# Kernel optimization log

Hardware: AMD Instinct MI355X
Metric: run time of the kernel (lower is better)

Reference implementation:

```python
import jax, jax.numpy as jnp
import numpy as np
from jax.scipy.special import logsumexp

REG = 0.1
ITERS = 10
TEMP = 0.1
W = 0.5            # cross_domain_weight
NEG = -1000000.0   # mask fill value used by the torch module
EPS = 1e-12        # F.normalize eps


def setup_inputs() -> dict:
    key = jax.random.key(0)
    k1, k2, k3, k4, k5 = jax.random.split(key, 5)
    n, n_ex, m, L, h = 64, 4, 49, 32, 512
    x = jax.random.normal(k1, (n * n_ex, m, h), jnp.float32)
    y = jax.random.normal(k2, (n, L, h), jnp.float32)
    lengths = jax.random.randint(k3, (n,), 8, L + 1)
    y_mask = jnp.arange(L)[None, :] >= lengths[:, None]  # True = padded token
    dustbin_im = 0.1 * jax.random.normal(k4, (1, 1, 1), jnp.float32)
    dustbin_lang = 0.1 * jax.random.normal(k5, (1, 1, 1), jnp.float32)
    return {"x": x, "y": y, "dustbin_im": dustbin_im,
            "dustbin_lang": dustbin_lang, "y_mask": y_mask}


def _l2norm(t):
    return t / jnp.maximum(jnp.linalg.norm(t, axis=-1, keepdims=True), EPS)


def _log_sinkhorn(Z, log_mu, log_nu, mask_cols, iters, reg):
    # Z: (b, m+1, n+1); mask_cols: (b, n+1) bool, True = invalid column
    u = jnp.zeros_like(log_mu)
    v = jnp.where(mask_cols, NEG, jnp.zeros_like(log_nu))
    pen = mask_cols[:, None, :].astype(Z.dtype) * 1e6

    def body(carry, _):
        u, v = carry
        M = (Z + u[:, :, None] + v[:, None, :]) / reg
        u = u + reg * (log_mu - logsumexp(M, axis=2))
        M = (Z + u[:, :, None] + v[:, None, :]) / reg
        v_new = v + reg * (log_nu - logsumexp(M + pen, axis=1))
        v = jnp.where(mask_cols, NEG, v_new)
        return (u, v), None

    (u, v), _ = jax.lax.scan(body, (u, v), None, length=iters)
    return (Z + u[:, :, None] + v[:, None, :]) / reg


def reference(x, y, dustbin_im, dustbin_lang, y_mask):
    n, L, h = y.shape
    n_ex = x.shape[0] // n
    m = x.shape[1]
    b = n * n * n_ex

    xn = _l2norm(x)   # (n*n_ex, m, h)
    yn = _l2norm(y)   # (n, L, h)
    # equivalent to repeat_interleave(x, n) vs repeat(y, n*n_ex): index i*n + j
    scores = jnp.einsum('imh,jlh->ijml', xn, yn).reshape(b, m, L)

    mask_cols = jnp.tile(y_mask, (n * n_ex, 1))                       # (b, L)
    mask_cols = jnp.concatenate([mask_cols, jnp.zeros((b, 1), bool)], axis=1)  # (b, L+1)
    scores_mask = jnp.broadcast_to(mask_cols[:, None, :], (b, m + 1, L + 1))

    a_im = jnp.clip(dustbin_im, -1.0, 1.0)
    a_lang = jnp.clip(dustbin_lang, -1.0, 1.0)
    bins0 = jnp.broadcast_to(a_im, (b, m, 1))
    bins1 = jnp.broadcast_to(a_lang, (b, 1, L))
    alpha = jnp.broadcast_to(a_im, (b, 1, 1))
    couplings = jnp.concatenate(
        [jnp.concatenate([scores, bins0], axis=2),
         jnp.concatenate([bins1, alpha], axis=2)], axis=1)            # (b, m+1, L+1)
    couplings = jnp.where(scores_mask, NEG, couplings)

    ms = jnp.asarray(m, scores.dtype)
    ns = (~scores_mask).sum(axis=(1, 2)).astype(scores.dtype) / (m + 1) - 1  # valid tokens per row
    norm = -jnp.log(ms + ns)                                          # (b,)
    log_mu = jnp.concatenate(
        [jnp.broadcast_to(norm[:, None], (b, m)), (jnp.log(ns) + norm)[:, None]], axis=1)
    log_nu = jnp.concatenate(
        [jnp.broadcast_to(norm[:, None], (b, L)), (jnp.log(ms) + norm)[:, None]], axis=1)
    log_nu = jnp.where(mask_cols, NEG, log_nu)

    Zlog = _log_sinkhorn(couplings, log_mu, log_nu, mask_cols, ITERS, REG)
    Zm = jnp.exp(Zlog - norm[:, None, None])                          # transport plan
    ot_scores = (scores * Zm[:, :-1, :-1]).sum(axis=(1, 2)) / TEMP    # (b,)

    scores2 = ot_scores.reshape(n * n_ex, n)
    matching = Zm.reshape(n * n_ex, n, m + 1, L + 1)

    idx = jnp.arange(n * n_ex)
    grp = idx // n_ex                                                 # lang index of image i
    pos = scores2[idx, grp]                                           # (n*n_ex,)
    # InfoNCE by language: pos vs all other langs for each image (full row)
    loss_lang = -(pos - logsumexp(scores2, axis=1)).mean()
    # InfoNCE by image: pos vs out-of-group images for the same lang
    cols = scores2.T[grp]                                             # (n*n_ex, n*n_ex), row i = scores2[:, grp[i]]
    allowed = (idx[None, :] // n_ex != grp[:, None]) | (idx[None, :] == idx[:, None])
    lse_im = logsumexp(jnp.where(allowed, cols, -jnp.inf), axis=1)
    loss_im = -(pos - lse_im).mean()
    loss = W * loss_lang + (1.0 - W) * loss_im
    return matching, loss
```

## Files before the change

kernel.cpp:

```cpp
#include <hip/hip_runtime.h>
#include <math.h>

#define XROWS 12544
#define YROWS 2048
#define HD 512
#define NM 49
#define NL 32
#define MP1 50
#define LP1 33
#define BSTRIDE 1650
#define INVREG 10.0f
#define ZSTR 1652

typedef __attribute__((ext_vector_type(8))) short short8;
typedef __attribute__((ext_vector_type(4))) float floatx4;
typedef _Float16 half2_t __attribute__((ext_vector_type(2)));

__device__ __forceinline__ unsigned short f2bf(float f) {
    unsigned int u = __builtin_bit_cast(unsigned int, f);
    u = (u + 0x7FFFu + ((u >> 16) & 1u)) >> 16;
    return (unsigned short)u;
}
__device__ __forceinline__ unsigned short f16b(float v) {
    return __builtin_bit_cast(unsigned short, (_Float16)v);
}

__device__ __forceinline__ void gload_lds16(const void* g, void* l) {
    typedef const __attribute__((address_space(1))) unsigned int* gp_t;
    typedef __attribute__((address_space(3))) unsigned int* lp_t;
    __builtin_amdgcn_global_load_lds((gp_t)g, (lp_t)l, 16, 0, 0);
}

__device__ __forceinline__ float rl(float v, int l) {
    return __builtin_bit_cast(float, __builtin_amdgcn_readlane(__builtin_bit_cast(int, v), l));
}
__device__ __forceinline__ half2_t rlh2(unsigned v, int l) {
    return __builtin_bit_cast(half2_t, (unsigned)__builtin_amdgcn_readlane((int)v, l));
}
__device__ __forceinline__ float fdot2(half2_t a, half2_t b, float c) {
    return __builtin_amdgcn_fdot2(a, b, c, false);
}

__global__ __launch_bounds__(256) void normcvt_kernel(
    const float* __restrict__ x, const float* __restrict__ y,
    unsigned short* __restrict__ xb, unsigned short* __restrict__ yb)
{
    const int wid = blockIdx.x * 4 + (threadIdx.x >> 6);
    const int lane = threadIdx.x & 63;
    if (wid >= XROWS + YROWS) return;
    const float* src;
    unsigned short* dst;
    if (wid < XROWS) { src = x + (size_t)wid * HD;           dst = xb + (size_t)wid * HD; }
    else             { src = y + (size_t)(wid - XROWS) * HD; dst = yb + (size_t)(wid - XROWS) * HD; }
    const float4 v0 = *(const float4*)(src + lane * 8);
    const float4 v1 = *(const float4*)(src + lane * 8 + 4);
    float s = v0.x*v0.x + v0.y*v0.y + v0.z*v0.z + v0.w*v0.w
            + v1.x*v1.x + v1.y*v1.y + v1.z*v1.z + v1.w*v1.w;
    #pragma unroll
    for (int o = 32; o > 0; o >>= 1) s += __shfl_xor(s, o, 64);
    const float inv = 1.0f / fmaxf(sqrtf(s), 1e-12f);
    short8 ov;
    ov[0] = (short)f2bf(v0.x * inv); ov[1] = (short)f2bf(v0.y * inv);
    ov[2] = (short)f2bf(v0.z * inv); ov[3] = (short)f2bf(v0.w * inv);
    ov[4] = (short)f2bf(v1.x * inv); ov[5] = (short)f2bf(v1.y * inv);
    ov[6] = (short)f2bf(v1.z * inv); ov[7] = (short)f2bf(v1.w * inv);
    *(short8*)(dst + lane * 8) = ov;
}

__global__ __launch_bounds__(512) void fused_kernel(
    const unsigned short* __restrict__ xb, const unsigned short* __restrict__ yb,
    const int* __restrict__ ymask,
    const float* __restrict__ d_im, const float* __restrict__ d_lang,
    float* __restrict__ outZ, float* __restrict__ scores2)
{
    const int wv   = threadIdx.x >> 6;
    const int lane = threadIdx.x & 63;
    const int i  = blockIdx.x & 255;
    const int jg = blockIdx.x >> 8;
    const int j  = jg * 8 + wv;
    const int pair = i * 64 + j;
    __shared__ alignas(16) float LDSU[8 * ZSTR];
    char* XSB = (char*)LDSU;
    float* zs = LDSU + wv * ZSTR;
    float* base = outZ + (size_t)pair * BSTRIDE;

    #pragma unroll
    for (int pass = 0; pass < 7; ++pass) {
        const int row = pass * 8 + wv;
        if (row < NM)
            gload_lds16(xb + ((size_t)i * NM + row) * HD + lane * 8, XSB + row * 1040);
    }
    __syncthreads();

    const int mval = (lane < NL) ? (ymask[j * NL + lane] != 0) : 1;
    const unsigned long long vbm = __ballot(lane < NL && !mval);
    const float ns = (float)__popcll(vbm);
    const float kim   = __expf(fminf(fmaxf(d_im[0],   -1.f), 1.f) * INVREG);
    const float klang = __expf(fminf(fmaxf(d_lang[0], -1.f), 1.f) * INVREG);

    const int la = lane & 15;
    const int koff = (lane >> 4) * 8;
    const unsigned short* yr0 = yb + ((size_t)j * NL + la) * HD + koff;
    const unsigned short* yr1 = yr0 + 16 * HD;

    floatx4 acc[4][2] = {};
    #pragma unroll
    for (int kt = 0; kt < 16; ++kt) {
        const int kb = (kt * 32 + koff) * 2;
        const short8 a0 = *(const short8*)(XSB + (0  + la) * 1040 + kb);
        const short8 a1 = *(const short8*)(XSB + (16 + la) * 1040 + kb);
        const short8 a2 = *(const short8*)(XSB + (32 + la) * 1040 + kb);
        const short8 a3 = *(const short8*)(XSB + 48 * 1040 + kb);
        const short8 b0 = *(const short8*)(yr0 + kt * 32);
        const short8 b1 = *(const short8*)(yr1 + kt * 32);
        acc[0][0] = __builtin_amdgcn_mfma_f32_16x16x32_bf16(a0, b0, acc[0][0], 0, 0, 0);
        acc[0][1] = __builtin_amdgcn_mfma_f32_16x16x32_bf16(a0, b1, acc[0][1], 0, 0, 0);
        acc[1][0] = __builtin_amdgcn_mfma_f32_16x16x32_bf16(a1, b0, acc[1][0], 0, 0, 0);
        acc[1][1] = __builtin_amdgcn_mfma_f32_16x16x32_bf16(a1, b1, acc[1][1], 0, 0, 0);
        acc[2][0] = __builtin_amdgcn_mfma_f32_16x16x32_bf16(a2, b0, acc[2][0], 0, 0, 0);
        acc[2][1] = __builtin_amdgcn_mfma_f32_16x16x32_bf16(a2, b1, acc[2][1], 0, 0, 0);
        acc[3][0] = __builtin_amdgcn_mfma_f32_16x16x32_bf16(a3, b0, acc[3][0], 0, 0, 0);
        acc[3][1] = __builtin_amdgcn_mfma_f32_16x16x32_bf16(a3, b1, acc[3][1], 0, 0, 0);
    }
    __syncthreads();

    unsigned short* T = (unsigned short*)zs;
    const bool mA = (vbm >> la) & 1ull;
    const bool mB = (vbm >> (16 + la)) & 1ull;
    float kA[16], kB[16];
    #pragma unroll
    for (int mi = 0; mi < 3; ++mi)
        #pragma unroll
        for (int q = 0; q < 4; ++q) {
            kA[mi*4+q] = mA ? __expf(acc[mi][0][q] * INVREG) : 0.f;
            kB[mi*4+q] = mB ? __expf(acc[mi][1][q] * INVREG) : 0.f;
        }
    kA[12] = mA ? __expf(acc[3][0][0] * INVREG) : 0.f;
    kB[12] = mB ? __expf(acc[3][1][0] * INVREG) : 0.f;
    kA[13] = kA[14] = kA[15] = 0.f;
    kB[13] = kB[14] = kB[15] = 0.f;

    #pragma unroll
    for (int mi = 0; mi < 3; ++mi) {
        const int r0 = mi * 16 + ((lane >> 4) << 2);
        ushort4 wa, wb;
        wa.x = f16b(kA[mi*4+0]); wa.y = f16b(kA[mi*4+1]);
        wa.z = f16b(kA[mi*4+2]); wa.w = f16b(kA[mi*4+3]);
        wb.x = f16b(kB[mi*4+0]); wb.y = f16b(kB[mi*4+1]);
        wb.z = f16b(kB[mi*4+2]); wb.w = f16b(kB[mi*4+3]);
        *(ushort4*)(T + la * 52 + r0)        = wa;
        *(ushort4*)(T + (16 + la) * 52 + r0) = wb;
    }
    if ((lane >> 4) == 0) {
        T[la * 52 + 48]        = f16b(kA[12]);
        T[(16 + la) * 52 + 48] = f16b(kB[12]);
    }
    if (lane < NL)       T[lane * 52 + 49] = f16b(((vbm >> lane) & 1ull) ? klang : 0.f);
    else if (lane == NL) T[32 * 52 + 49]   = f16b(kim);
    if (lane < NM)       T[32 * 52 + lane] = f16b(kim);
    asm volatile("s_waitcnt lgkmcnt(0)" ::: "memory");
    __builtin_amdgcn_sched_barrier(0);

    half2_t kr2[17];
    {
        const int p = (lane < MP1) ? lane : 0;
        #pragma unroll
        for (int q = 0; q < 16; ++q) {
            const unsigned lo = T[(2*q)   * 52 + p];
            const unsigned hi = T[(2*q+1) * 52 + p];
            kr2[q] = __builtin_bit_cast(half2_t, lo | (hi << 16));
        }
        half2_t h; h[0] = (_Float16)kim; h[1] = (_Float16)0.f;
        kr2[16] = h;
    }
    half2_t kc2[25];
    {
        const int tb = ((lane < LP1) ? lane : 0) * 52;
        #pragma unroll
        for (int q = 0; q < 25; ++q)
            kc2[q] = __builtin_bit_cast(half2_t, *(const unsigned*)(T + tb + 2*q));
    }

    const float mup = (lane < NM) ? 1.f : ns;
    const float nup = (lane < NL) ? 1.f : 49.f;
    const bool colA = (lane < NL) ? (((vbm >> lane) & 1ull) != 0ull) : (lane == NL);
    float eu = 0.f;
    float ev = colA ? 1.f : 0.f;

    for (int it = 0; it < 10; ++it) {
        const float evn = __shfl_xor(ev, 1, 64);
        const auto evp_ = __builtin_amdgcn_cvt_pkrtz(ev, evn);
        const unsigned evpu = __builtin_bit_cast(unsigned, evp_);
        float a0 = 0.f, a1 = 0.f;
        #pragma unroll
        for (int q = 0; q < 17; q += 2) {
            a0 = fdot2(kr2[q], rlh2(evpu, 2*q), a0);
            if (q + 1 < 17) a1 = fdot2(kr2[q+1], rlh2(evpu, 2*q+2), a1);
        }
        eu = __fdividef(mup, a0 + a1);

        const float eun = __shfl_xor(eu, 1, 64);
        const auto eup_ = __builtin_amdgcn_cvt_pkrtz(eu, eun);
        const unsigned eupu = __builtin_bit_cast(unsigned, eup_);
        float b0 = 0.f, b1 = 0.f;
        #pragma unroll
        for (int q = 0; q < 25; q += 2) {
            b0 = fdot2(kc2[q], rlh2(eupu, 2*q), b0);
            if (q + 1 < 25) b1 = fdot2(kc2[q+1], rlh2(eupu, 2*q+2), b1);
        }
        const float Sv = b0 + b1;
        ev = colA ? __fdividef(nup, Sv) : 0.f;
    }

    const float ev32 = rl(ev, 32);
    const float eu49 = rl(eu, 49);
    const float evA  = __shfl(ev, la, 64);
    const float evB  = __shfl(ev, 16 + la, 64);
    float ot = 0.f;
    #pragma unroll
    for (int mi = 0; mi < 4; ++mi) {
        #pragma unroll
        for (int q = 0; q < 4; ++q) {
            const int row = mi * 16 + ((lane >> 4) << 2) + q;
            const float eur = __shfl(eu, row, 64);
            if (row < NM) {
                const float s0 = acc[mi][0][q];
                const float s1 = acc[mi][1][q];
                const float zm0 = kA[mi*4+q] * eur * evA;
                const float zm1 = kB[mi*4+q] * eur * evB;
                zs[row * 33 + la]      = zm0;
                zs[row * 33 + 16 + la] = zm1;
                ot = fmaf(s0 * INVREG, zm0, fmaf(s1 * INVREG, zm1, ot));
            }
        }
    }
    if (lane < MP1) zs[lane * 33 + 32] = kim * eu * ev32;
    if (lane < LP1) {
        const float kd = (lane < NL) ? (((vbm >> lane) & 1ull) ? klang : 0.f) : kim;
        zs[NM * 33 + lane] = kd * eu49 * ev;
    }
    #pragma unroll
    for (int o = 32; o > 0; o >>= 1) ot += __shfl_xor(ot, o, 64);
    if (lane == 0) scores2[pair] = ot;
    asm volatile("s_waitcnt lgkmcnt(0)" ::: "memory");
    __builtin_amdgcn_sched_barrier(0);
    #pragma unroll
    for (int t = 0; t < 13; ++t) {
        const int idx = t * 64 + lane;
        if (idx < 825) *(float2*)(base + idx * 2) = *(const float2*)&zs[idx * 2];
    }
}

__global__ __launch_bounds__(256) void loss_kernel(
    const float* __restrict__ s2, float* __restrict__ out)
{
    __shared__ float S2[16384];
    __shared__ float colmax[64], colsum[64];
    __shared__ float wred[4];
    const int tid = threadIdx.x;
    for (int t = tid; t < 4096; t += 256)
        ((float4*)S2)[t] = ((const float4*)s2)[t];
    __syncthreads();

    const int gc = tid >> 2, sc = tid & 3;
    float cm = -3.0e38f;
    for (int k = sc * 64; k < sc * 64 + 64; ++k) cm = fmaxf(cm, S2[k * 64 + gc]);
    cm = fmaxf(cm, __shfl_xor(cm, 1, 64));
    cm = fmaxf(cm, __shfl_xor(cm, 2, 64));
    float cs = 0.f;
    for (int k = sc * 64; k < sc * 64 + 64; ++k)
        if ((k >> 2) != gc) cs += __expf(S2[k * 64 + gc] - cm);
    cs += __shfl_xor(cs, 1, 64);
    cs += __shfl_xor(cs, 2, 64);
    if (sc == 0) { colmax[gc] = cm; colsum[gc] = cs; }
    __syncthreads();

    const int i = tid;
    const int g = i >> 2;
    const float pos = S2[i * 64 + g];
    float mx = -3.0e38f;
    for (int jj = 0; jj < 64; ++jj) {
        const int c = (jj + i) & 63;
        mx = fmaxf(mx, S2[i * 64 + c]);
    }
    float sm = 0.f;
    for (int jj = 0; jj < 64; ++jj) {
        const int c = (jj + i) & 63;
        sm += __expf(S2[i * 64 + c] - mx);
    }
    const float lse1 = __logf(sm) + mx;

    const float cmg = colmax[g], csg = colsum[g];
    const float lse2 = __logf(csg + __expf(pos - cmg)) + cmg;

    float li = 0.5f * (lse1 - pos) + 0.5f * (lse2 - pos);
    #pragma unroll
    for (int o = 32; o > 0; o >>= 1) li += __shfl_xor(li, o, 64);
    if ((i & 63) == 0) wred[i >> 6] = li;
    __syncthreads();
    if (i == 0) out[0] = (wred[0] + wred[1] + wred[2] + wred[3]) * (1.0f / 256.0f);
}

extern "C" void kernel_launch(void* const* d_in, const int* in_sizes, int n_in,
                              void* d_out, int out_size, void* d_ws, size_t ws_size,
                              hipStream_t stream)
{
    const float* x      = (const float*)d_in[0];
    const float* y      = (const float*)d_in[1];
    const float* d_im   = (const float*)d_in[2];
    const float* d_lang = (const float*)d_in[3];
    const int* ymask    = (const int*)d_in[4];
    float* out = (float*)d_out;
    float* ws  = (float*)d_ws;

    float* s2          = ws;
    unsigned short* xb = (unsigned short*)(ws + 16384);
    unsigned short* yb = xb + (size_t)XROWS * HD;

    normcvt_kernel<<<(XROWS + YROWS + 3) / 4, 256, 0, stream>>>(x, y, xb, yb);
    fused_kernel<<<2048, 512, 0, stream>>>(xb, yb, ymask, d_im, d_lang, out, s2);
    loss_kernel<<<1, 256, 0, stream>>>(s2, out + (size_t)16384 * BSTRIDE);
}
```

Measured before the change: 145.5 us.

## Drop LDS staging of x tiles and transport plan, use direct global access

Result: slower. 192.7 us (+32.5%).

```diff
diff --git a/kernel.cpp b/kernel.cpp
--- a/kernel.cpp
+++ b/kernel.cpp
@@ -10,7 +10,6 @@
 #define LP1 33
 #define BSTRIDE 1650
 #define INVREG 10.0f
-#define ZSTR 1652
 
 typedef __attribute__((ext_vector_type(8))) short short8;
 typedef __attribute__((ext_vector_type(4))) float floatx4;
@@ -23,12 +22,6 @@
 }
 __device__ __forceinline__ unsigned short f16b(float v) {
     return __builtin_bit_cast(unsigned short, (_Float16)v);
-}
-
-__device__ __forceinline__ void gload_lds16(const void* g, void* l) {
-    typedef const __attribute__((address_space(1))) unsigned int* gp_t;
-    typedef __attribute__((address_space(3))) unsigned int* lp_t;
-    __builtin_amdgcn_global_load_lds((gp_t)g, (lp_t)l, 16, 0, 0);
 }
 
 __device__ __forceinline__ float rl(float v, int l) {
@@ -79,18 +72,9 @@
     const int jg = blockIdx.x >> 8;
     const int j  = jg * 8 + wv;
     const int pair = i * 64 + j;
-    __shared__ alignas(16) float LDSU[8 * ZSTR];
-    char* XSB = (char*)LDSU;
-    float* zs = LDSU + wv * ZSTR;
+    __shared__ alignas(16) unsigned short TAll[8][1728];
+    unsigned short* T = TAll[wv];
     float* base = outZ + (size_t)pair * BSTRIDE;
-
-    #pragma unroll
-    for (int pass = 0; pass < 7; ++pass) {
-        const int row = pass * 8 + wv;
-        if (row < NM)
-            gload_lds16(xb + ((size_t)i * NM + row) * HD + lane * 8, XSB + row * 1040);
-    }
-    __syncthreads();
 
     const int mval = (lane < NL) ? (ymask[j * NL + lane] != 0) : 1;
     const unsigned long long vbm = __ballot(lane < NL && !mval);
@@ -100,19 +84,23 @@
 
     const int la = lane & 15;
     const int koff = (lane >> 4) * 8;
+    const unsigned short* xr0 = xb + ((size_t)i * NM + la) * HD + koff;
+    const unsigned short* xr1 = xr0 + 16 * HD;
+    const unsigned short* xr2 = xr0 + 32 * HD;
+    const unsigned short* xr3 = xb + ((size_t)i * NM + 48) * HD + koff;
     const unsigned short* yr0 = yb + ((size_t)j * NL + la) * HD + koff;
     const unsigned short* yr1 = yr0 + 16 * HD;
 
     floatx4 acc[4][2] = {};
     #pragma unroll
     for (int kt = 0; kt < 16; ++kt) {
-        const int kb = (kt * 32 + koff) * 2;
-        const short8 a0 = *(const short8*)(XSB + (0  + la) * 1040 + kb);
-        const short8 a1 = *(const short8*)(XSB + (16 + la) * 1040 + kb);
-        const short8 a2 = *(const short8*)(XSB + (32 + la) * 1040 + kb);
-        const short8 a3 = *(const short8*)(XSB + 48 * 1040 + kb);
-        const short8 b0 = *(const short8*)(yr0 + kt * 32);
-        const short8 b1 = *(const short8*)(yr1 + kt * 32);
+        const int k0 = kt * 32;
+        const short8 a0 = *(const short8*)(xr0 + k0);
+        const short8 a1 = *(const short8*)(xr1 + k0);
+        const short8 a2 = *(const short8*)(xr2 + k0);
+        const short8 a3 = *(const short8*)(xr3 + k0);
+        const short8 b0 = *(const short8*)(yr0 + k0);
+        const short8 b1 = *(const short8*)(yr1 + k0);
         acc[0][0] = __builtin_amdgcn_mfma_f32_16x16x32_bf16(a0, b0, acc[0][0], 0, 0, 0);
         acc[0][1] = __builtin_amdgcn_mfma_f32_16x16x32_bf16(a0, b1, acc[0][1], 0, 0, 0);
         acc[1][0] = __builtin_amdgcn_mfma_f32_16x16x32_bf16(a1, b0, acc[1][0], 0, 0, 0);
@@ -122,38 +110,27 @@
         acc[3][0] = __builtin_amdgcn_mfma_f32_16x16x32_bf16(a3, b0, acc[3][0], 0, 0, 0);
         acc[3][1] = __builtin_amdgcn_mfma_f32_16x16x32_bf16(a3, b1, acc[3][1], 0, 0, 0);
     }
-    __syncthreads();
-
-    unsigned short* T = (unsigned short*)zs;
+
     const bool mA = (vbm >> la) & 1ull;
     const bool mB = (vbm >> (16 + la)) & 1ull;
-    float kA[16], kB[16];
-    #pragma unroll
-    for (int mi = 0; mi < 3; ++mi)
-        #pragma unroll
-        for (int q = 0; q < 4; ++q) {
-            kA[mi*4+q] = mA ? __expf(acc[mi][0][q] * INVREG) : 0.f;
-            kB[mi*4+q] = mB ? __expf(acc[mi][1][q] * INVREG) : 0.f;
-        }
-    kA[12] = mA ? __expf(acc[3][0][0] * INVREG) : 0.f;
-    kB[12] = mB ? __expf(acc[3][1][0] * INVREG) : 0.f;
-    kA[13] = kA[14] = kA[15] = 0.f;
-    kB[13] = kB[14] = kB[15] = 0.f;
-
     #pragma unroll
     for (int mi = 0; mi < 3; ++mi) {
         const int r0 = mi * 16 + ((lane >> 4) << 2);
         ushort4 wa, wb;
-        wa.x = f16b(kA[mi*4+0]); wa.y = f16b(kA[mi*4+1]);
-        wa.z = f16b(kA[mi*4+2]); wa.w = f16b(kA[mi*4+3]);
-        wb.x = f16b(kB[mi*4+0]); wb.y = f16b(kB[mi*4+1]);
-        wb.z = f16b(kB[mi*4+2]); wb.w = f16b(kB[mi*4+3]);
+        wa.x = f16b(mA ? __expf(acc[mi][0][0] * INVREG) : 0.f);
+        wa.y = f16b(mA ? __expf(acc[mi][0][1] * INVREG) : 0.f);
+        wa.z = f16b(mA ? __expf(acc[mi][0][2] * INVREG) : 0.f);
+        wa.w = f16b(mA ? __expf(acc[mi][0][3] * INVREG) : 0.f);
+        wb.x = f16b(mB ? __expf(acc[mi][1][0] * INVREG) : 0.f);
+        wb.y = f16b(mB ? __expf(acc[mi][1][1] * INVREG) : 0.f);
+        wb.z = f16b(mB ? __expf(acc[mi][1][2] * INVREG) : 0.f);
+        wb.w = f16b(mB ? __expf(acc[mi][1][3] * INVREG) : 0.f);
         *(ushort4*)(T + la * 52 + r0)        = wa;
         *(ushort4*)(T + (16 + la) * 52 + r0) = wb;
     }
     if ((lane >> 4) == 0) {
-        T[la * 52 + 48]        = f16b(kA[12]);
-        T[(16 + la) * 52 + 48] = f16b(kB[12]);
+        T[la * 52 + 48]        = f16b(mA ? __expf(acc[3][0][0] * INVREG) : 0.f);
+        T[(16 + la) * 52 + 48] = f16b(mB ? __expf(acc[3][1][0] * INVREG) : 0.f);
     }
     if (lane < NL)       T[lane * 52 + 49] = f16b(((vbm >> lane) & 1ull) ? klang : 0.f);
     else if (lane == NL) T[32 * 52 + 49]   = f16b(kim);
@@ -189,8 +166,8 @@
 
     for (int it = 0; it < 10; ++it) {
         const float evn = __shfl_xor(ev, 1, 64);
-        const auto evp_ = __builtin_amdgcn_cvt_pkrtz(ev, evn);
-        const unsigned evpu = __builtin_bit_cast(unsigned, evp_);
+        half2_t evp; evp[0] = (_Float16)ev; evp[1] = (_Float16)evn;
+        const unsigned evpu = __builtin_bit_cast(unsigned, evp);
         float a0 = 0.f, a1 = 0.f;
         #pragma unroll
         for (int q = 0; q < 17; q += 2) {
@@ -200,8 +177,8 @@
         eu = __fdividef(mup, a0 + a1);
 
         const float eun = __shfl_xor(eu, 1, 64);
-        const auto eup_ = __builtin_amdgcn_cvt_pkrtz(eu, eun);
-        const unsigned eupu = __builtin_bit_cast(unsigned, eup_);
+        half2_t eup; eup[0] = (_Float16)eu; eup[1] = (_Float16)eun;
+        const unsigned eupu = __builtin_bit_cast(unsigned, eup);
         float b0 = 0.f, b1 = 0.f;
         #pragma unroll
         for (int q = 0; q < 25; q += 2) {
@@ -226,29 +203,22 @@
             if (row < NM) {
                 const float s0 = acc[mi][0][q];
                 const float s1 = acc[mi][1][q];
-                const float zm0 = kA[mi*4+q] * eur * evA;
-                const float zm1 = kB[mi*4+q] * eur * evB;
-                zs[row * 33 + la]      = zm0;
-                zs[row * 33 + 16 + la] = zm1;
+                const float zm0 = __expf(s0 * INVREG) * eur * evA;
+                const float zm1 = __expf(s1 * INVREG) * eur * evB;
+                base[row * 33 + la]      = zm0;
+                base[row * 33 + 16 + la] = zm1;
                 ot = fmaf(s0 * INVREG, zm0, fmaf(s1 * INVREG, zm1, ot));
             }
         }
     }
-    if (lane < MP1) zs[lane * 33 + 32] = kim * eu * ev32;
+    if (lane < MP1) base[lane * 33 + 32] = kim * eu * ev32;
     if (lane < LP1) {
         const float kd = (lane < NL) ? (((vbm >> lane) & 1ull) ? klang : 0.f) : kim;
-        zs[NM * 33 + lane] = kd * eu49 * ev;
+        base[NM * 33 + lane] = kd * eu49 * ev;
     }
     #pragma unroll
     for (int o = 32; o > 0; o >>= 1) ot += __shfl_xor(ot, o, 64);
     if (lane == 0) scores2[pair] = ot;
-    asm volatile("s_waitcnt lgkmcnt(0)" ::: "memory");
-    __builtin_amdgcn_sched_barrier(0);
-    #pragma unroll
-    for (int t = 0; t < 13; ++t) {
-        const int idx = t * 64 + lane;
-        if (idx < 825) *(float2*)(base + idx * 2) = *(const float2*)&zs[idx * 2];
-    }
 }
 
 __global__ __launch_bounds__(256) void loss_kernel(
```
